# Optimization experiments

Measured on AMD Instinct MI355X. Metric: run time of the kernel, lower is better.

The kernel has to match this reference:

```python
import jax, jax.numpy as jnp
import numpy as np

B = 2048   # batch of sampled occupation configurations
L = 64     # nphysical (spatial orbitals / MPS sites)
P = 4      # local physical dimension (2 spin orbitals -> 4 occupations)
D = 128    # MPS bond dimension


def setup_inputs() -> dict:
    key = jax.random.key(0)
    k1, k2, k3, k4 = jax.random.split(key, 4)
    onstate = jax.random.randint(k1, (B, L), 0, P)  # occupation per site
    # flat MPS data buffer reshaped to [site, occupation, Dl, Dr];
    # scale by D**-0.5 so the length-L matrix chain stays O(1).
    site_tensors = jax.random.normal(k2, (L, P, D, D), dtype=jnp.float32) * (D ** -0.5)
    left_vec = jax.random.normal(k3, (D,), dtype=jnp.float32)
    right_vec = jax.random.normal(k4, (D,), dtype=jnp.float32)
    return {
        "onstate": onstate,
        "site_tensors": site_tensors,
        "left_vec": left_vec,
        "right_vec": right_vec,
    }


def reference(onstate, site_tensors, right_vec, left_vec=None, **_ignore):
    # keyword-robust shim not needed; real signature below
    raise NotImplementedError


def reference(onstate, site_tensors, left_vec, right_vec):
    """MPS amplitude: amp[b] = l^T (prod_i A[i, s_{b,i}]) r, evaluated as a
    left-to-right chain of gathered batched vector-matrix products."""
    batch = onstate.shape[0]
    s_seq = onstate.T.astype(jnp.int32)                      # [L, B]
    v0 = jnp.broadcast_to(left_vec, (batch, left_vec.shape[0]))  # [B, D]

    def step(v, inp):
        A_i, s_i = inp            # A_i: [P, D, D], s_i: [B]
        M = A_i[s_i]              # data-dependent gather -> [B, D, D]
        v = jnp.einsum('bd,bde->be', v, M)
        return v, None

    vL, _ = jax.lax.scan(step, v0, (site_tensors, s_seq))
    return vL @ right_vec         # [B] amplitudes
```

## Files before the change

### kernel.cpp

```cpp
#include <hip/hip_runtime.h>
#include <hip/hip_fp16.h>

constexpr int L = 64;
constexpr int P = 4;
constexpr int D = 128;
constexpr int B = 2048;
constexpr int EPW = 16;
constexpr int NG = B / EPW;

using v8h = __attribute__((ext_vector_type(8))) _Float16;
using v4h = __attribute__((ext_vector_type(4))) _Float16;
using v4f = __attribute__((ext_vector_type(4))) float;

constexpr size_t UT_OFF  = 0;
constexpr size_t WT_OFF  = 1048576;
constexpr size_t MTF_OFF = 2097152;
constexpr size_t MTB_OFF = 6291456;

constexpr int VLDS0 = 131072;
constexpr int VLDS1 = 131072 + 4096;
constexpr int PLDS  = 131072 + 8192;
constexpr int SMEM_BYTES = PLDS + L * EPW * 4;

#define WAIT_VM8   0xF78
#define WAIT_VM0   0xF70
#define WAIT_LGKM0 0xC07F

__device__ __forceinline__ void gl2lds16(const void* g, void* l) {
  __builtin_amdgcn_global_load_lds(
      (const __attribute__((address_space(1))) void*)g,
      (__attribute__((address_space(3))) void*)l, 16, 0, 0);
}

__global__ void convert_dual(const float* __restrict__ src,
                             _Float16* __restrict__ mtf,
                             _Float16* __restrict__ mtb) {
  const int mat = blockIdx.x;
  const int site = mat >> 2;
  const int t = threadIdx.x;
  if (site >= 32) {
    const float4* sb = (const float4*)(src + (size_t)mat * 16384);
    _Float16* bb = mtb + (size_t)(mat - 128) * 16384;
#pragma unroll
    for (int it = 0; it < 16; ++it) {
      int idx = t + it * 256;
      float4 f = sb[idx];
      v4h h4 = {(_Float16)f.x, (_Float16)f.y, (_Float16)f.z, (_Float16)f.w};
      *(v4h*)(bb + idx * 4) = h4;
    }
    return;
  }
  const float* sb = src + (size_t)mat * 16384;
  _Float16* fb = mtf + (size_t)mat * 16384;
  const int cl = t & 63;
  const int dg = t >> 6;
#pragma unroll
  for (int ch = 0; ch < 2; ++ch) {
    const int c = ch * 64 + cl;
#pragma unroll
    for (int dh = 0; dh < 4; ++dh) {
      const int d8 = dh * 4 + dg;
      v8h v;
#pragma unroll
      for (int j = 0; j < 8; ++j) v[j] = (_Float16)sb[(d8 * 8 + j) * D + c];
      *(v8h*)(fb + c * D + d8 * 8) = v;
    }
  }
}

__global__ __launch_bounds__(512, 1) void mps_half_chain(
    const int* __restrict__ onstate, const _Float16* __restrict__ mtf,
    const _Float16* __restrict__ mtb, const float* __restrict__ left_vec,
    const float* __restrict__ right_vec, float* __restrict__ ut,
    float* __restrict__ wt) {
  extern __shared__ char smem[];
  const int tid = threadIdx.x;
  const int wave = tid >> 6, lane = tid & 63;
  const int me = lane & 15, q4 = lane >> 4;
  const bool fwd = !(blockIdx.x & 1);
  const int b0 = (blockIdx.x >> 1) * EPW;
  const _Float16* mbase = fwd ? mtf : mtb;
  const float* ivec = fwd ? left_vec : right_vec;
  float* ovec = fwd ? ut : wt;

  int* plds = (int*)(smem + PLDS);
#pragma unroll
  for (int j = 0; j < 2; ++j) {
    int idx = tid + j * 512;
    int e = idx >> 6, i = idx & 63;
    plds[i * EPW + e] = onstate[(b0 + e) * L + i];
  }
  if (tid < 256) {
    int e = tid >> 4, seg = tid & 15;
    _Float16* vp = (_Float16*)(smem + VLDS0) + e * 128 + (seg ^ (e & 7)) * 8;
#pragma unroll
    for (int j = 0; j < 8; ++j) vp[j] = (_Float16)ivec[seg * 8 + j];
  }

  char* wbuf = smem + wave * 16384;

  int soff[8];
#pragma unroll
  for (int i = 0; i < 8; ++i) {
    int u = i * 64 + lane;
    int p = u >> 7, r = u & 127, cl = r >> 3, slot = r & 7;
    soff[i] = p * 32768 + (wave * 16 + cl) * 256 + (slot ^ (cl & 7)) * 16;
  }
  auto stage = [&](int ls, int h, int z) {
    const char* gb = (const char*)mbase + (size_t)ls * 131072 + h * 128;
    char* lb = wbuf + z * 8192;
#pragma unroll
    for (int i = 0; i < 8; ++i) gl2lds16(gb + soff[i], lb + i * 1024);
  };
  auto consume = [&](int h, int z, int pm, const char* vb, v4f& acc) {
    const int s0 = h * 8 + q4, s1 = h * 8 + 4 + q4;
    v8h a0 = *(const v8h*)(vb + me * 256 + (s0 ^ (me & 7)) * 16);
    v8h a1 = *(const v8h*)(vb + me * 256 + (s1 ^ (me & 7)) * 16);
    const char* cb = wbuf + z * 8192;
#pragma unroll
    for (int p = 0; p < P; ++p) {
      const bool isp = (pm == p);
      v8h zf = {};
      v8h am0 = isp ? a0 : zf;
      v8h am1 = isp ? a1 : zf;
      const char* pb = cb + p * 2048 + me * 128;
      v8h bf0 = *(const v8h*)(pb + ((q4) ^ (me & 7)) * 16);
      v8h bf1 = *(const v8h*)(pb + ((4 + q4) ^ (me & 7)) * 16);
      acc = __builtin_amdgcn_mfma_f32_16x16x32_f16(am0, bf0, acc, 0, 0, 0);
      acc = __builtin_amdgcn_mfma_f32_16x16x32_f16(am1, bf1, acc, 0, 0, 0);
    }
  };

  stage(fwd ? 0 : 31, 0, 0);
  __syncthreads();

  const int c0 = wave * 16 + me;
  v4f accL = {0.f, 0.f, 0.f, 0.f};
  for (int site = 0; site < 32; ++site) {
    const int site_g = fwd ? site : 63 - site;
    const int ls     = fwd ? site : 31 - site;
    const int pm = plds[site_g * EPW + me];
    const char* vb = smem + ((site & 1) ? VLDS1 : VLDS0);
    v4f acc = {0.f, 0.f, 0.f, 0.f};

    stage(ls, 1, 1);
    consume(0, 0, pm, vb, acc);

    if (site < 31) {
      const int lsn = fwd ? site + 1 : 30 - site;
      __builtin_amdgcn_sched_barrier(0);
      __builtin_amdgcn_s_waitcnt(WAIT_LGKM0);
      __builtin_amdgcn_sched_barrier(0);
      stage(lsn, 0, 0);
      __builtin_amdgcn_s_waitcnt(WAIT_VM8);
      consume(1, 1, pm, vb, acc);
      _Float16* vn = (_Float16*)(smem + ((site & 1) ? VLDS0 : VLDS1));
#pragma unroll
      for (int r = 0; r < 4; ++r) {
        int e = q4 * 4 + r;
        vn[e * 128 + ((c0 >> 3) ^ (e & 7)) * 8 + (c0 & 7)] = (_Float16)acc[r];
      }
      __syncthreads();
    } else {
      __builtin_amdgcn_s_waitcnt(WAIT_VM0);
      consume(1, 1, pm, vb, acc);
      accL = acc;
    }
  }
#pragma unroll
  for (int r = 0; r < 4; ++r) ovec[c0 * B + b0 + q4 * 4 + r] = accL[r];
}

__global__ void combine_uw(const float* __restrict__ ut,
                           const float* __restrict__ wt,
                           float* __restrict__ out) {
  const int b = blockIdx.x * 256 + threadIdx.x;
  float s = 0.f;
#pragma unroll 8
  for (int d = 0; d < D; ++d) s += ut[d * B + b] * wt[d * B + b];
  out[b] = s;
}

extern "C" void kernel_launch(void* const* d_in, const int* in_sizes, int n_in,
                              void* d_out, int out_size, void* d_ws,
                              size_t ws_size, hipStream_t stream) {
  const int*   onstate      = (const int*)d_in[0];
  const float* site_tensors = (const float*)d_in[1];
  const float* left_vec     = (const float*)d_in[2];
  const float* right_vec    = (const float*)d_in[3];
  float*       out          = (float*)d_out;
  char*        ws           = (char*)d_ws;
  float*       ut           = (float*)(ws + UT_OFF);
  float*       wt           = (float*)(ws + WT_OFF);
  _Float16*    mtf          = (_Float16*)(ws + MTF_OFF);
  _Float16*    mtb          = (_Float16*)(ws + MTB_OFF);

  hipFuncSetAttribute((const void*)mps_half_chain,
                      hipFuncAttributeMaxDynamicSharedMemorySize, SMEM_BYTES);

  convert_dual<<<L * P, 256, 0, stream>>>(site_tensors, mtf, mtb);
  mps_half_chain<<<2 * NG, 512, SMEM_BYTES, stream>>>(
      onstate, mtf, mtb, left_vec, right_vec, ut, wt);
  combine_uw<<<B / 256, 256, 0, stream>>>(ut, wt, out);
}
```

Baseline: 132.3 us.

## Fuse convert, chain and combine into one cooperative kernel with grid syncs

Merges the fp16 conversion, the half-chain MFMA kernel and the final dot-product combine into one cooperative launch of 256 blocks. Grid-wide syncs with thread fences replace the kernel boundaries. The aim is to remove two kernel launch gaps. In exchange it adds grid-sync overhead, and it depends on all 256 blocks (one per CU, large LDS) being co-resident, which cooperative launch requires.

```diff
diff --git a/kernel.cpp b/kernel.cpp
--- a/kernel.cpp
+++ b/kernel.cpp
@@ -1,12 +1,14 @@
 #include <hip/hip_runtime.h>
 #include <hip/hip_fp16.h>
+#include <hip/hip_cooperative_groups.h>
+
+namespace cg = cooperative_groups;
 
 constexpr int L = 64;
 constexpr int P = 4;
 constexpr int D = 128;
 constexpr int B = 2048;
 constexpr int EPW = 16;
-constexpr int NG = B / EPW;
 
 using v8h = __attribute__((ext_vector_type(8))) _Float16;
 using v4h = __attribute__((ext_vector_type(4))) _Float16;
@@ -32,51 +34,55 @@
       (__attribute__((address_space(3))) void*)l, 16, 0, 0);
 }
 
-__global__ void convert_dual(const float* __restrict__ src,
-                             _Float16* __restrict__ mtf,
-                             _Float16* __restrict__ mtb) {
-  const int mat = blockIdx.x;
-  const int site = mat >> 2;
-  const int t = threadIdx.x;
-  if (site >= 32) {
-    const float4* sb = (const float4*)(src + (size_t)mat * 16384);
-    _Float16* bb = mtb + (size_t)(mat - 128) * 16384;
-#pragma unroll
-    for (int it = 0; it < 16; ++it) {
-      int idx = t + it * 256;
-      float4 f = sb[idx];
-      v4h h4 = {(_Float16)f.x, (_Float16)f.y, (_Float16)f.z, (_Float16)f.w};
-      *(v4h*)(bb + idx * 4) = h4;
-    }
-    return;
-  }
-  const float* sb = src + (size_t)mat * 16384;
-  _Float16* fb = mtf + (size_t)mat * 16384;
-  const int cl = t & 63;
-  const int dg = t >> 6;
-#pragma unroll
-  for (int ch = 0; ch < 2; ++ch) {
-    const int c = ch * 64 + cl;
-#pragma unroll
-    for (int dh = 0; dh < 4; ++dh) {
-      const int d8 = dh * 4 + dg;
-      v8h v;
-#pragma unroll
-      for (int j = 0; j < 8; ++j) v[j] = (_Float16)sb[(d8 * 8 + j) * D + c];
-      *(v8h*)(fb + c * D + d8 * 8) = v;
-    }
-  }
-}
-
-__global__ __launch_bounds__(512, 1) void mps_half_chain(
-    const int* __restrict__ onstate, const _Float16* __restrict__ mtf,
-    const _Float16* __restrict__ mtb, const float* __restrict__ left_vec,
-    const float* __restrict__ right_vec, float* __restrict__ ut,
-    float* __restrict__ wt) {
+__global__ __launch_bounds__(512, 1) void mps_fused(
+    const float* __restrict__ src, const int* __restrict__ onstate,
+    const float* __restrict__ left_vec, const float* __restrict__ right_vec,
+    float* __restrict__ out, char* __restrict__ ws) {
+  float*    ut  = (float*)(ws + UT_OFF);
+  float*    wt  = (float*)(ws + WT_OFF);
+  _Float16* mtf = (_Float16*)(ws + MTF_OFF);
+  _Float16* mtb = (_Float16*)(ws + MTB_OFF);
+
   extern __shared__ char smem[];
   const int tid = threadIdx.x;
   const int wave = tid >> 6, lane = tid & 63;
   const int me = lane & 15, q4 = lane >> 4;
+
+  {
+    const int mat = blockIdx.x;
+    const int site = mat >> 2;
+    if (site >= 32) {
+      const float4* sb = (const float4*)(src + (size_t)mat * 16384);
+      _Float16* bb = mtb + (size_t)(mat - 128) * 16384;
+#pragma unroll
+      for (int it = 0; it < 8; ++it) {
+        int idx = tid + it * 512;
+        float4 f = sb[idx];
+        v4h h4 = {(_Float16)f.x, (_Float16)f.y, (_Float16)f.z, (_Float16)f.w};
+        *(v4h*)(bb + idx * 4) = h4;
+      }
+    } else {
+      const float* sb = src + (size_t)mat * 16384;
+      _Float16* fb = mtf + (size_t)mat * 16384;
+      const int cl = tid & 63;
+      const int dg = tid >> 6;
+#pragma unroll
+      for (int ch = 0; ch < 2; ++ch) {
+        const int c = ch * 64 + cl;
+#pragma unroll
+        for (int dh = 0; dh < 2; ++dh) {
+          const int d8 = dh * 8 + dg;
+          v8h v;
+#pragma unroll
+          for (int j = 0; j < 8; ++j) v[j] = (_Float16)sb[(d8 * 8 + j) * D + c];
+          *(v8h*)(fb + c * D + d8 * 8) = v;
+        }
+      }
+    }
+  }
+  __threadfence();
+  cg::this_grid().sync();
+
   const bool fwd = !(blockIdx.x & 1);
   const int b0 = (blockIdx.x >> 1) * EPW;
   const _Float16* mbase = fwd ? mtf : mtb;
@@ -169,16 +175,17 @@
   }
 #pragma unroll
   for (int r = 0; r < 4; ++r) ovec[c0 * B + b0 + q4 * 4 + r] = accL[r];
-}
-
-__global__ void combine_uw(const float* __restrict__ ut,
-                           const float* __restrict__ wt,
-                           float* __restrict__ out) {
-  const int b = blockIdx.x * 256 + threadIdx.x;
-  float s = 0.f;
+
+  __threadfence();
+  cg::this_grid().sync();
+
+  if (blockIdx.x < 4) {
+    const int b = blockIdx.x * 512 + tid;
+    float s = 0.f;
 #pragma unroll 8
-  for (int d = 0; d < D; ++d) s += ut[d * B + b] * wt[d * B + b];
-  out[b] = s;
+    for (int d = 0; d < D; ++d) s += ut[d * B + b] * wt[d * B + b];
+    out[b] = s;
+  }
 }
 
 extern "C" void kernel_launch(void* const* d_in, const int* in_sizes, int n_in,
@@ -190,16 +197,12 @@
   const float* right_vec    = (const float*)d_in[3];
   float*       out          = (float*)d_out;
   char*        ws           = (char*)d_ws;
-  float*       ut           = (float*)(ws + UT_OFF);
-  float*       wt           = (float*)(ws + WT_OFF);
-  _Float16*    mtf          = (_Float16*)(ws + MTF_OFF);
-  _Float16*    mtb          = (_Float16*)(ws + MTB_OFF);
-
-  hipFuncSetAttribute((const void*)mps_half_chain,
+
+  hipFuncSetAttribute((const void*)mps_fused,
                       hipFuncAttributeMaxDynamicSharedMemorySize, SMEM_BYTES);
 
-  convert_dual<<<L * P, 256, 0, stream>>>(site_tensors, mtf, mtb);
-  mps_half_chain<<<2 * NG, 512, SMEM_BYTES, stream>>>(
-      onstate, mtf, mtb, left_vec, right_vec, ut, wt);
-  combine_uw<<<B / 256, 256, 0, stream>>>(ut, wt, out);
+  void* args[] = {(void*)&site_tensors, (void*)&onstate, (void*)&left_vec,
+                  (void*)&right_vec,    (void*)&out,     (void*)&ws};
+  hipLaunchCooperativeKernel((const void*)mps_fused, dim3(256), dim3(512),
+                             args, SMEM_BYTES, stream);
 }
```

Measured after the change: 329.9 us. +149.3%, slower.
